# Kernel tuning notes

Measured on AMD Instinct MI355X. Metric: run time of the kernel, lower is better.

Reference implementation:

```python
import jax, jax.numpy as jnp
import numpy as np

B, S, D, H, DFF, NB = 32, 512, 256, 8, 1024, 2
L = NB + 2 * NB  # 2 blocks_1 + 4 blocks_2 = 6 layers, params stacked on axis 0
DK = D // H
NEG = jnp.float32(-1e32)


def _ln(x, s, b):
    mu = jnp.mean(x, -1, keepdims=True)
    var = jnp.mean((x - mu) ** 2, -1, keepdims=True)
    return (x - mu) * jax.lax.rsqrt(var + 1e-5) * s + b


def _attn(q, k, v, gamma, mask, zero_pad):
    # q,k,v: [B,H,S,DK]; mask: [1,1,S,S] bool; gamma: [H,1,1]
    scores = jnp.einsum('bhid,bhjd->bhij', q, k) / jnp.float32(np.sqrt(DK))
    # distance-decay effect (computed with no grad in the original)
    sc = jax.nn.softmax(jnp.where(mask, scores, NEG), axis=-1) * mask
    cum = jnp.cumsum(sc, axis=-1)
    tot = jnp.sum(sc, axis=-1, keepdims=True)
    idx = jnp.arange(S, dtype=jnp.float32)
    pos = jnp.abs(idx[None, :] - idx[:, None])[None, None]  # |i-j|
    dist = jax.lax.stop_gradient(jnp.sqrt(jnp.maximum((tot - cum) * pos, 0.0)))
    g = -jax.nn.softplus(gamma)[None]  # [1,H,1,1]
    eff = jnp.clip(jnp.exp(dist * g), 1e-5, 1e5)
    scores = jnp.where(mask, scores * eff, NEG)
    a = jax.nn.softmax(scores, axis=-1)
    if zero_pad:
        a = a.at[:, :, 0, :].set(0.0)
    return jnp.einsum('bhij,bhjd->bhid', a, v)


def _layer(i, mask_flag, q, k, v, apply_pos,
           Wk, bk, Wv, bv, Wo, bo, gammas, ln1_s, ln1_b, W1, b1, W2, b2, ln2_s, ln2_b):
    diag = 0 if mask_flag == 1 else -1  # mask=1: incl. diag; mask=0: strictly past
    mask = jnp.tril(jnp.ones((S, S), bool), diag)[None, None]
    to_h = lambda x, W, bb: (x @ W + bb).reshape(B, S, H, DK).transpose(0, 2, 1, 3)
    qh = to_h(q, Wk[i], bk[i])  # kq_same=True -> q uses k_linear
    kh = to_h(k, Wk[i], bk[i])
    vh = to_h(v, Wv[i], bv[i])
    o = _attn(qh, kh, vh, gammas[i], mask, zero_pad=(mask_flag == 0))
    o = o.transpose(0, 2, 1, 3).reshape(B, S, D) @ Wo[i] + bo[i]
    q = _ln(q + o, ln1_s[i], ln1_b[i])
    if apply_pos:
        f = jax.nn.relu(q @ W1[i] + b1[i]) @ W2[i] + b2[i]
        q = _ln(q + f, ln2_s[i], ln2_b[i])
    return q


def _forward(q_embed_data, qa_embed_data, *p):
    y, x = qa_embed_data, q_embed_data
    for i in range(NB):
        y = _layer(i, 1, y, y, y, True, *p)
    flag = True
    for j in range(2 * NB):
        i = NB + j
        if flag:
            x = _layer(i, 1, x, x, x, False, *p)
        else:
            x = _layer(i, 0, x, x, y, True, *p)
        flag = not flag
    return x


def setup_inputs() -> dict:
    key = jax.random.key(0)
    ks = jax.random.split(key, 9)
    sd = jnp.float32(1.0 / np.sqrt(D))
    sdf = jnp.float32(1.0 / np.sqrt(DFF))
    xb = float(np.sqrt(3.0))  # xavier bound for gammas (fan_in=fan_out=1)
    return {
        'q_embed_data': jax.random.normal(ks[0], (B, S, D), jnp.float32),
        'qa_embed_data': jax.random.normal(ks[1], (B, S, D), jnp.float32),
        'Wk': jax.random.normal(ks[2], (L, D, D), jnp.float32) * sd,
        'bk': jnp.zeros((L, D), jnp.float32),
        'Wv': jax.random.normal(ks[3], (L, D, D), jnp.float32) * sd,
        'bv': jnp.zeros((L, D), jnp.float32),
        'Wo': jax.random.normal(ks[4], (L, D, D), jnp.float32) * sd,
        'bo': jnp.zeros((L, D), jnp.float32),
        'gammas': jax.random.uniform(ks[5], (L, H, 1, 1), jnp.float32, -xb, xb),
        'ln1_s': jnp.ones((L, D), jnp.float32),
        'ln1_b': jnp.zeros((L, D), jnp.float32),
        'W1': jax.random.normal(ks[6], (L, D, DFF), jnp.float32) * sd,
        'b1': jnp.zeros((L, DFF), jnp.float32),
        'W2': jax.random.normal(ks[7], (L, DFF, D), jnp.float32) * sdf,
        'b2': jnp.zeros((L, D), jnp.float32),
        'ln2_s': jnp.ones((L, D), jnp.float32),
        'ln2_b': jnp.zeros((L, D), jnp.float32),
    }


def reference(q_embed_data, qa_embed_data, Wk, bk, Wv, bv, Wo, bo, gammas,
              ln1_s, ln1_b, W1, b1, W2, b2, ln2_s, ln2_b):
    return _forward(q_embed_data, qa_embed_data, Wk, bk, Wv, bv, Wo, bo, gammas,
                    ln1_s, ln1_b, W1, b1, W2, b2, ln2_s, ln2_b)
```

## Files before the change

### kernel.cpp

```cpp
#include <hip/hip_runtime.h>
#include <cstdint>
#include <cstddef>


#define AS1 __attribute__((address_space(1)))
#define AS3 __attribute__((address_space(3)))

typedef __bf16 bf16;
typedef __bf16 bf16x8 __attribute__((ext_vector_type(8)));
typedef __bf16 bf16x4 __attribute__((ext_vector_type(4)));
typedef __bf16 bf16x2 __attribute__((ext_vector_type(2)));
typedef float  f32x4  __attribute__((ext_vector_type(4)));
typedef float  f32x16 __attribute__((ext_vector_type(16)));
typedef unsigned int u32;

static constexpr int Mc = 32 * 512;

__global__ void cvt_copy2_kernel(const float* __restrict__ s0, float* __restrict__ da32,
                                 bf16* __restrict__ da16, const float* __restrict__ s1,
                                 float* __restrict__ db32, bf16* __restrict__ db16, int n4) {
  const float* s = blockIdx.y ? s1 : s0;
  float* d32 = blockIdx.y ? db32 : da32;
  bf16* d16 = blockIdx.y ? db16 : da16;
  int i = blockIdx.x * blockDim.x + threadIdx.x;
  if (i < n4) {
    float4 v = ((const float4*)s)[i];
    ((float4*)d32)[i] = v;
    bf16x4 hx = {(bf16)v.x, (bf16)v.y, (bf16)v.z, (bf16)v.w};
    ((bf16x4*)d16)[i] = hx;
  }
}

__global__ __launch_bounds__(256) void transpose_cvt_all(
    const float* __restrict__ Wk, const float* __restrict__ Wv, const float* __restrict__ Wo,
    const float* __restrict__ W1, const float* __restrict__ W2,
    bf16* __restrict__ Wkt, bf16* __restrict__ Wvt, bf16* __restrict__ Wot,
    bf16* __restrict__ W1t, bf16* __restrict__ W2t) {
  int z = blockIdx.z;
  int layer = z % 6, w = z / 6;
  const float* src; bf16* dst; int K, N;
  switch (w) {
    case 0: src = Wk; dst = Wkt; K = 256; N = 256; break;
    case 1: src = Wv; dst = Wvt; K = 256; N = 256; break;
    case 2: src = Wo; dst = Wot; K = 256; N = 256; break;
    case 3: src = W1; dst = W1t; K = 256; N = 1024; break;
    default: src = W2; dst = W2t; K = 1024; N = 256; break;
  }
  int k0 = blockIdx.x * 64, n0 = blockIdx.y * 64;
  if (k0 >= K || n0 >= N) return;
  src += (size_t)layer * K * N;
  dst += (size_t)layer * K * N;
  __shared__ bf16 t[64][68];
  int tid = threadIdx.x;
  int rr = tid >> 4;
  int c4 = (tid & 15) * 4;
#pragma unroll
  for (int p = 0; p < 4; ++p) {
    int k = rr + p * 16;
    float4 v = *(const float4*)(src + (size_t)(k0 + k) * N + n0 + c4);
    t[c4 + 0][k] = (bf16)v.x;
    t[c4 + 1][k] = (bf16)v.y;
    t[c4 + 2][k] = (bf16)v.z;
    t[c4 + 3][k] = (bf16)v.w;
  }
  __syncthreads();
#pragma unroll
  for (int p = 0; p < 4; ++p) {
    int nl = rr + p * 16;
    bf16x4 o4 = *(const bf16x4*)&t[nl][c4];
    *(bf16x4*)(dst + (size_t)(n0 + nl) * K + k0 + c4) = o4;
  }
}

template <int RELU, typename OUT_T>
__device__ __forceinline__ void gemm_body(
    const bf16* __restrict__ A, const bf16* __restrict__ Bt,
    const float* __restrict__ bias, OUT_T* __restrict__ C,
    int K, int N, int m0, int n0, bf16* As, bf16* Bs) {
  const int tid = threadIdx.x;
  const int lane = tid & 63;
  const int wid = tid >> 6;
  const int wm = (wid >> 1) * 64;
  const int wn = (wid & 1) * 64;
  f32x4 acc[4][4] = {};

  const int o1 = wid * 1024 + lane * 16;
  const int o2 = o1 + 4096;
  const int r1 = o1 >> 6, c1 = o1 & 63;
  const int r2 = o2 >> 6, c2 = o2 & 63;
  const char* Ab = (const char*)A;
  const char* Bb = (const char*)Bt;
  const size_t stride = (size_t)K * 2;

  auto stage_panel = [&](int panel, int kk) {
    const char* a1 = Ab + (size_t)(m0 + r1) * stride + (size_t)kk * 2 + c1;
    const char* a2 = Ab + (size_t)(m0 + r2) * stride + (size_t)kk * 2 + c2;
    const char* b1 = Bb + (size_t)(n0 + r1) * stride + (size_t)kk * 2 + c1;
    const char* b2 = Bb + (size_t)(n0 + r2) * stride + (size_t)kk * 2 + c2;
    char* ad = (char*)As + panel * 8192 + wid * 1024;
    char* bd = (char*)Bs + panel * 8192 + wid * 1024;
    __builtin_amdgcn_global_load_lds((const AS1 u32*)a1, (AS3 u32*)ad, 16, 0, 0);
    __builtin_amdgcn_global_load_lds((const AS1 u32*)a2, (AS3 u32*)(ad + 4096), 16, 0, 0);
    __builtin_amdgcn_global_load_lds((const AS1 u32*)b1, (AS3 u32*)bd, 16, 0, 0);
    __builtin_amdgcn_global_load_lds((const AS1 u32*)b2, (AS3 u32*)(bd + 4096), 16, 0, 0);
  };

  stage_panel(0, 0);
  stage_panel(1, 32);
  asm volatile("s_waitcnt vmcnt(0)" ::: "memory");
  __syncthreads();

  int cur = 0;
  for (int k0 = 0; k0 < K; k0 += 64) {
    if (k0 + 64 < K) {
      stage_panel((cur ^ 1) * 2, k0 + 64);
      stage_panel((cur ^ 1) * 2 + 1, k0 + 96);
    }
    const int rr = lane & 15;
    const int g8 = (lane >> 4) * 8;
#pragma unroll
    for (int s = 0; s < 2; ++s) {
      const int base = (cur * 2 + s) * 4096;
      bf16x8 af[4], bfr[4];
#pragma unroll
      for (int i = 0; i < 4; ++i) {
        af[i]  = *(const bf16x8*)&As[base + (wm + i * 16 + rr) * 32 + g8];
        bfr[i] = *(const bf16x8*)&Bs[base + (wn + i * 16 + rr) * 32 + g8];
      }
#pragma unroll
      for (int mi = 0; mi < 4; ++mi)
#pragma unroll
        for (int ni = 0; ni < 4; ++ni)
          acc[mi][ni] = __builtin_amdgcn_mfma_f32_16x16x32_bf16(af[mi], bfr[ni], acc[mi][ni], 0, 0, 0);
    }
    asm volatile("s_waitcnt vmcnt(0)" ::: "memory");
    __syncthreads();
    cur ^= 1;
  }

  const int rr = lane & 15;
  const int g4 = (lane >> 4) * 4;
  float bv[4];
#pragma unroll
  for (int ni = 0; ni < 4; ++ni) bv[ni] = bias[n0 + wn + ni * 16 + rr];
#pragma unroll
  for (int mi = 0; mi < 4; ++mi)
#pragma unroll
    for (int ni = 0; ni < 4; ++ni)
#pragma unroll
      for (int r = 0; r < 4; ++r) {
        float v = acc[mi][ni][r] + bv[ni];
        if (RELU) v = fmaxf(v, 0.f);
        int row = m0 + wm + mi * 16 + g4 + r;
        int col = n0 + wn + ni * 16 + rr;
        C[(size_t)row * N + col] = (OUT_T)v;
      }
}

template <int RELU, typename OUT_T>
__global__ __launch_bounds__(256) void gemm_bias_kernel(
    const bf16* __restrict__ A, const bf16* __restrict__ Bt,
    const float* __restrict__ bias, OUT_T* __restrict__ C, int K, int N) {
  __shared__ bf16 As[4 * 4096];
  __shared__ bf16 Bs[4 * 4096];
  gemm_body<RELU, OUT_T>(A, Bt, bias, C, K, N, blockIdx.x * 128, blockIdx.y * 128, As, Bs);
}

__global__ __launch_bounds__(256) void gemm_kv_kernel(
    const bf16* __restrict__ A0, const bf16* __restrict__ Bt0,
    const float* __restrict__ b0, bf16* __restrict__ C0,
    const bf16* __restrict__ A1, const bf16* __restrict__ Bt1,
    const float* __restrict__ b1, bf16* __restrict__ C1, int K, int N) {
  __shared__ bf16 As[4 * 4096];
  __shared__ bf16 Bs[4 * 4096];
  int sel = blockIdx.y >> 1;
  gemm_body<0, bf16>(sel ? A1 : A0, sel ? Bt1 : Bt0, sel ? b1 : b0, sel ? C1 : C0,
                     K, N, blockIdx.x * 128, (blockIdx.y & 1) * 128, As, Bs);
}

template <int KSZ>
__global__ __launch_bounds__(512, 4) void gemm_ln_kernel(
    const bf16* __restrict__ A, const bf16* __restrict__ Bt,
    const float* __restrict__ bias, const float* __restrict__ resid,
    const float* __restrict__ lns, const float* __restrict__ lnb,
    float* __restrict__ out32, bf16* __restrict__ out16) {
  __shared__ bf16 As[2 * 32 * 32];
  __shared__ bf16 Bs[2 * 256 * 32];
  __shared__ float wsum[8][16][2];
  __shared__ float stats[32][2];
  const int tid = threadIdx.x, lane = tid & 63, wid = tid >> 6;
  const int m0 = blockIdx.x * 32;
  const int wr = wid >> 2, wc = wid & 3;
  f32x4 acc[4] = {};
  const char* Ab = (const char*)A;
  const char* Bb = (const char*)Bt;
  const size_t stride = (size_t)KSZ * 2;

  auto stage = [&](int buf, int kk) {
    if (wid < 2) {
      int off = wid * 1024 + lane * 16;
      const char* a1 = Ab + (size_t)(m0 + (off >> 6)) * stride + (size_t)kk * 2 + (off & 63);
      __builtin_amdgcn_global_load_lds((const AS1 u32*)a1,
                                       (AS3 u32*)((char*)As + buf * 2048 + wid * 1024), 16, 0, 0);
    }
    int off1 = wid * 2048 + lane * 16;
    int off2 = off1 + 1024;
    const char* b1 = Bb + (size_t)(off1 >> 6) * stride + (size_t)kk * 2 + (off1 & 63);
    const char* b2 = Bb + (size_t)(off2 >> 6) * stride + (size_t)kk * 2 + (off2 & 63);
    char* bd = (char*)Bs + buf * 16384 + wid * 2048;
    __builtin_amdgcn_global_load_lds((const AS1 u32*)b1, (AS3 u32*)bd, 16, 0, 0);
    __builtin_amdgcn_global_load_lds((const AS1 u32*)b2, (AS3 u32*)(bd + 1024), 16, 0, 0);
  };

  stage(0, 0);
  asm volatile("s_waitcnt vmcnt(0)" ::: "memory");
  __syncthreads();

  int cur = 0;
  for (int k0 = 0; k0 < KSZ; k0 += 32) {
    if (k0 + 32 < KSZ) stage(cur ^ 1, k0 + 32);
    const int rr = lane & 15, g8 = (lane >> 4) * 8;
    bf16x8 af = *(const bf16x8*)&As[cur * 1024 + (wr * 16 + rr) * 32 + g8];
    bf16x8 bfr[4];
#pragma unroll
    for (int ni = 0; ni < 4; ++ni)
      bfr[ni] = *(const bf16x8*)&Bs[cur * 8192 + (wc * 64 + ni * 16 + rr) * 32 + g8];
#pragma unroll
    for (int ni = 0; ni < 4; ++ni)
      acc[ni] = __builtin_amdgcn_mfma_f32_16x16x32_bf16(af, bfr[ni], acc[ni], 0, 0, 0);
    asm volatile("s_waitcnt vmcnt(0)" ::: "memory");
    __syncthreads();
    cur ^= 1;
  }

  const int rr = lane & 15, g4 = (lane >> 4) * 4;
  float bv[4], scv[4], biv[4];
  int col[4];
#pragma unroll
  for (int ni = 0; ni < 4; ++ni) {
    col[ni] = wc * 64 + ni * 16 + rr;
    bv[ni] = bias[col[ni]];
    scv[ni] = lns[col[ni]];
    biv[ni] = lnb[col[ni]];
  }
  float v[4][4];
#pragma unroll
  for (int r = 0; r < 4; ++r) {
    int grow = m0 + wr * 16 + g4 + r;
#pragma unroll
    for (int ni = 0; ni < 4; ++ni)
      v[ni][r] = acc[ni][r] + bv[ni] + resid[(size_t)grow * 256 + col[ni]];
  }
#pragma unroll
  for (int r = 0; r < 4; ++r) {
    float s1 = (v[0][r] + v[1][r]) + (v[2][r] + v[3][r]);
    float s2 = (v[0][r] * v[0][r] + v[1][r] * v[1][r]) + (v[2][r] * v[2][r] + v[3][r] * v[3][r]);
#pragma unroll
    for (int off = 8; off; off >>= 1) {
      s1 += __shfl_xor(s1, off);
      s2 += __shfl_xor(s2, off);
    }
    if (rr == 0) {
      int lrow = wr * 16 + g4 + r;
      wsum[wid][lrow & 15][0] = s1;
      wsum[wid][lrow & 15][1] = s2;
    }
  }
  __syncthreads();
  if (tid < 32) {
    int row = tid;
    int band = row >> 4;
    float s1 = 0.f, s2 = 0.f;
#pragma unroll
    for (int k = 0; k < 4; ++k) {
      s1 += wsum[band * 4 + k][row & 15][0];
      s2 += wsum[band * 4 + k][row & 15][1];
    }
    float mu = s1 * (1.f / 256.f);
    float var = s2 * (1.f / 256.f) - mu * mu;
    stats[row][0] = mu;
    stats[row][1] = rsqrtf(var + 1e-5f);
  }
  __syncthreads();
#pragma unroll
  for (int r = 0; r < 4; ++r) {
    int lrow = wr * 16 + g4 + r;
    int grow = m0 + lrow;
    float mu = stats[lrow][0], rs = stats[lrow][1];
#pragma unroll
    for (int ni = 0; ni < 4; ++ni) {
      float y = (v[ni][r] - mu) * rs * scv[ni] + biv[ni];
      out32[(size_t)grow * 256 + col[ni]] = y;
      out16[(size_t)grow * 256 + col[ni]] = (bf16)y;
    }
  }
}

static constexpr int LDK = 34;
static constexpr int LDV = 534;
static constexpr float LOG2E = 1.4426950408889634f;
static constexpr float KSC = 0.17677669529663687f * LOG2E;

__device__ __forceinline__ int jloc(int r, int hi) { return (r & 3) + 8 * (r >> 2) + 4 * hi; }

__device__ __forceinline__ u32 pkbf(float x, float y) {
  bf16x2 t = {(bf16)x, (bf16)y};
  return __builtin_bit_cast(u32, t);
}

__device__ __forceinline__ void plswap(u32& a, u32& b) {
  asm volatile("v_permlane32_swap_b32 %0, %1" : "+v"(a), "+v"(b));
}

__device__ __forceinline__ f32x16 qk_tile(const bf16* Klds, int jbase, int lq,
                                          const bf16x8& qf0, const bf16x8& qf1, int hi) {
  const bf16x8 ka0 = *(const bf16x8*)&Klds[(jbase + lq) * LDK + hi * 8];
  const bf16x8 ka1 = *(const bf16x8*)&Klds[(jbase + lq) * LDK + 16 + hi * 8];
  f32x16 c = {};
  c = __builtin_amdgcn_mfma_f32_32x32x16_bf16(ka0, qf0, c, 0, 0, 0);
  c = __builtin_amdgcn_mfma_f32_32x32x16_bf16(ka1, qf1, c, 0, 0, 0);
  return c;
}

template <bool MASKED>
__device__ __forceinline__ void tileA(const f32x16& c, int jbase, int hi, int qlim, float& tot) {
  float t[4] = {0.f, 0.f, 0.f, 0.f};
#pragma unroll
  for (int q2 = 0; q2 < 4; ++q2)
#pragma unroll
    for (int p = 0; p < 4; ++p) {
      const int r = q2 * 4 + p;
      float e = __builtin_amdgcn_exp2f(c[r] * KSC);
      if (MASKED) {
        int j = jbase + 8 * q2 + 4 * hi + p;
        if (j > qlim) e = 0.f;
      }
      t[q2] += e;
    }
  tot += (t[0] + t[1]) + (t[2] + t[3]);
}

template <bool MASKED>
__device__ __forceinline__ void tileB(const f32x16& c, int jbase, int lq, int hi,
                                      int qlim, float itot, float gneg2, float posf,
                                      const bf16* Vt, float& run, float& sum2, f32x16& pvacc) {
  float su2[16], lcs[16], G[4];
#pragma unroll
  for (int q2 = 0; q2 < 4; ++q2) {
    float a = 0.f;
#pragma unroll
    for (int p = 0; p < 4; ++p) {
      const int r = q2 * 4 + p;
      su2[r] = c[r] * KSC;
      float e = __builtin_amdgcn_exp2f(su2[r]);
      if (MASKED) {
        int j = jbase + 8 * q2 + 4 * hi + p;
        if (j > qlim) e = 0.f;
      }
      a += e;
      lcs[r] = a;
    }
    G[q2] = a;
  }
  float Po[4];
#pragma unroll
  for (int q2 = 0; q2 < 4; ++q2) Po[q2] = __shfl_xor(G[q2], 32);
  float base[4];
  {
    float pre = run;
#pragma unroll
    for (int q2 = 0; q2 < 4; ++q2) {
      base[q2] = pre + (hi ? Po[q2] : 0.f);
      pre += G[q2] + Po[q2];
    }
    run = pre;
  }
#pragma unroll
  for (int cc = 0; cc < 2; ++cc) {
    float pv[8];
#pragma unroll
    for (int q2s = 0; q2s < 2; ++q2s) {
      const int q2 = cc * 2 + q2s;
#pragma unroll
      for (int p = 0; p < 4; ++p) {
        const int r = q2 * 4 + p;
        float cum = base[q2] + lcs[r];
        float pos = posf - (float)(8 * q2 + p);
        float d2 = fmaxf(__builtin_fmaf(-cum, itot, 1.f) * pos, 0.f);
        float dist = __builtin_amdgcn_sqrtf(d2);
        float eff = fmaxf(__builtin_amdgcn_exp2f(dist * gneg2), 1e-5f);
        float t = __builtin_amdgcn_exp2f(su2[r] * eff);
        if (MASKED) {
          int j = jbase + 8 * q2 + 4 * hi + p;
          if (j > qlim) t = 0.f;
        }
        pv[q2s * 4 + p] = t;
      }
    }
    sum2 += ((pv[0] + pv[1]) + (pv[2] + pv[3])) + ((pv[4] + pv[5]) + (pv[6] + pv[7]));
    u32 a0 = pkbf(pv[0], pv[1]);
    u32 a1 = pkbf(pv[2], pv[3]);
    u32 b0 = pkbf(pv[4], pv[5]);
    u32 b1 = pkbf(pv[6], pv[7]);
    plswap(a0, b0);
    plswap(a1, b1);
    uint4 fq; fq.x = a0; fq.y = a1; fq.z = b0; fq.w = b1;
    bf16x8 pa = __builtin_bit_cast(bf16x8, fq);
    bf16x8 vb = *(const bf16x8*)&Vt[(size_t)lq * LDV + jbase + cc * 16 + hi * 8];
    pvacc = __builtin_amdgcn_mfma_f32_32x32x16_bf16(pa, vb, pvacc, 0, 0, 0);
  }
}

__global__ __launch_bounds__(1024, 4) void attn_kernel(
    const bf16* __restrict__ kh, const bf16* __restrict__ vh,
    const float* __restrict__ gam, bf16* __restrict__ o, int incl_diag) {
  __shared__ bf16 Klds[512 * LDK];
  __shared__ bf16 Vt[32 * LDV];
  __shared__ float exA[8][32];
  __shared__ float exB[8][32];
  __shared__ float s2A[8][32];
  __shared__ float pvp[8][32][32];

  const int tid = threadIdx.x;
  const int lane = tid & 63;
  const int wid = tid >> 6;
  const int bh = blockIdx.x;
  const int b = bh >> 3, h = bh & 7;
  const bf16* kbase = kh + ((size_t)b * 4096 + h) * 32;
  const bf16* vbase = vh + ((size_t)b * 4096 + h) * 32;
  bf16* obase = o + ((size_t)b * 4096 + h) * 32;

#pragma unroll
  for (int it = 0; it < 2; ++it) {
    int t = it * 1024 + tid;
    int j = t >> 2, cc = t & 3;
    bf16x8 kv8 = *(const bf16x8*)(kbase + (size_t)j * 256 + cc * 8);
    *(bf16x8*)&Klds[j * LDK + cc * 8] = kv8;
  }
  {
    int u = tid & 255;
    int cg = tid >> 8;
    const bf16* vb = vbase + (size_t)(2 * u) * 256 + cg * 8;
    bf16x8 r0 = *(const bf16x8*)(vb);
    bf16x8 r1 = *(const bf16x8*)(vb + 256);
#pragma unroll
    for (int e = 0; e < 8; ++e) {
      bf16x2 w2 = {r0[e], r1[e]};
      *(bf16x2*)&Vt[(size_t)(cg * 8 + e) * LDV + 2 * u] = w2;
    }
  }
  __syncthreads();

  float gm = gam[h];
  float gneg = -(fmaxf(gm, 0.f) + log1pf(__expf(-fabsf(gm))));
  const float gneg2 = gneg * LOG2E;
  const int lq = lane & 31;
  const int hi = lane >> 5;

  const int p = wid & 7;
  const bool front = wid < 8;
  const int f = 7 - p;
  const int qbHi = 15 - p;
  const int ntHi = 16 - p;
  const int q0Hi = qbHi * 32;
  const int qrHi = q0Hi + lq;
  const int qlimHi = incl_diag ? qrHi : qrHi - 1;
  const int q0Lo = p * 32;
  const int qrLo = q0Lo + lq;
  const int qlimLo = incl_diag ? qrLo : qrLo - 1;

  const bf16x8 qfH0 = *(const bf16x8*)&Klds[(q0Hi + lq) * LDK + hi * 8];
  const bf16x8 qfH1 = *(const bf16x8*)&Klds[(q0Hi + lq) * LDK + 16 + hi * 8];

  float totLo = 0.f, S = 0.f;
  if (front) {
    const bf16x8 qfL0 = *(const bf16x8*)&Klds[(q0Lo + lq) * LDK + hi * 8];
    const bf16x8 qfL1 = *(const bf16x8*)&Klds[(q0Lo + lq) * LDK + 16 + hi * 8];
    for (int jt = 0; jt < p; ++jt) {
      f32x16 c = qk_tile(Klds, jt * 32, lq, qfL0, qfL1, hi);
      tileA<false>(c, jt * 32, hi, qlimLo, totLo);
    }
    {
      f32x16 c = qk_tile(Klds, q0Lo, lq, qfL0, qfL1, hi);
      tileA<true>(c, q0Lo, hi, qlimLo, totLo);
    }
    totLo += __shfl_xor(totLo, 32);
    for (int jt = 0; jt < f; ++jt) {
      f32x16 c = qk_tile(Klds, jt * 32, lq, qfH0, qfH1, hi);
      tileA<false>(c, jt * 32, hi, qlimHi, S);
    }
    S += __shfl_xor(S, 32);
    if (lane < 32) exA[p][lq] = S;
  } else {
    for (int jt = f; jt < ntHi - 1; ++jt) {
      f32x16 c = qk_tile(Klds, jt * 32, lq, qfH0, qfH1, hi);
      tileA<false>(c, jt * 32, hi, qlimHi, S);
    }
    {
      f32x16 c = qk_tile(Klds, q0Hi, lq, qfH0, qfH1, hi);
      tileA<true>(c, q0Hi, hi, qlimHi, S);
    }
    S += __shfl_xor(S, 32);
    if (lane < 32) exB[p][lq] = S;
  }
  __syncthreads();
  const float SA = exA[p][lq];
  const float SB = exB[p][lq];
  const float totHi = SA + SB;
  const float itotHi = totHi > 0.f ? 1.f / totHi : 0.f;

  f32x16 pvHi = {};
  float sum2Hi = 0.f;
  if (front) {
    const bf16x8 qfL0 = *(const bf16x8*)&Klds[(q0Lo + lq) * LDK + hi * 8];
    const bf16x8 qfL1 = *(const bf16x8*)&Klds[(q0Lo + lq) * LDK + 16 + hi * 8];
    const float itotLo = totLo > 0.f ? 1.f / totLo : 0.f;
    f32x16 pvLo = {};
    float sum2Lo = 0.f, run = 0.f;
    float posf = (float)(qrLo - 4 * hi);
    for (int jt = 0; jt < p; ++jt) {
      f32x16 c = qk_tile(Klds, jt * 32, lq, qfL0, qfL1, hi);
      tileB<false>(c, jt * 32, lq, hi, qlimLo, itotLo, gneg2, posf, Vt, run, sum2Lo, pvLo);
      posf -= 32.f;
    }
    {
      f32x16 c = qk_tile(Klds, q0Lo, lq, qfL0, qfL1, hi);
      tileB<true>(c, q0Lo, lq, hi, qlimLo, itotLo, gneg2, posf, Vt, run, sum2Lo, pvLo);
    }
    sum2Lo += __shfl_xor(sum2Lo, 32);
    const float inv2Lo = sum2Lo > 0.f ? 1.f / sum2Lo : 0.f;
#pragma unroll
    for (int r = 0; r < 16; ++r) {
      int qv = jloc(r, hi);
      float iv = __shfl(inv2Lo, qv);
      obase[(size_t)(q0Lo + qv) * 256 + lq] = (bf16)(pvLo[r] * iv);
    }
    run = 0.f;
    posf = (float)(qrHi - 4 * hi);
    for (int jt = 0; jt < f; ++jt) {
      f32x16 c = qk_tile(Klds, jt * 32, lq, qfH0, qfH1, hi);
      tileB<false>(c, jt * 32, lq, hi, qlimHi, itotHi, gneg2, posf, Vt, run, sum2Hi, pvHi);
      posf -= 32.f;
    }
    sum2Hi += __shfl_xor(sum2Hi, 32);
    if (lane < 32) s2A[p][lq] = sum2Hi;
#pragma unroll
    for (int r = 0; r < 16; ++r) pvp[p][jloc(r, hi)][lq] = pvHi[r];
  } else {
    float run = SA;
    float posf = (float)(qrHi - 4 * hi - 32 * f);
    for (int jt = f; jt < ntHi - 1; ++jt) {
      f32x16 c = qk_tile(Klds, jt * 32, lq, qfH0, qfH1, hi);
      tileB<false>(c, jt * 32, lq, hi, qlimHi, itotHi, gneg2, posf, Vt, run, sum2Hi, pvHi);
      posf -= 32.f;
    }
    {
      f32x16 c = qk_tile(Klds, q0Hi, lq, qfH0, qfH1, hi);
      tileB<true>(c, q0Hi, lq, hi, qlimHi, itotHi, gneg2, posf, Vt, run, sum2Hi, pvHi);
    }
    sum2Hi += __shfl_xor(sum2Hi, 32);
  }
  __syncthreads();
  if (!front) {
    const float s2 = s2A[p][lq] + sum2Hi;
    const float inv2 = s2 > 0.f ? 1.f / s2 : 0.f;
#pragma unroll
    for (int r = 0; r < 16; ++r) {
      int qv = jloc(r, hi);
      float iv = __shfl(inv2, qv);
      float val = pvHi[r] + pvp[p][qv][lq];
      obase[(size_t)(q0Hi + qv) * 256 + lq] = (bf16)(val * iv);
    }
  }
}

extern "C" void kernel_launch(void* const* d_in, const int* in_sizes, int n_in,
                              void* d_out, int out_size, void* d_ws, size_t ws_size,
                              hipStream_t stream) {
  const float* q_embed  = (const float*)d_in[0];
  const float* qa_embed = (const float*)d_in[1];
  const float* Wk = (const float*)d_in[2];
  const float* bk = (const float*)d_in[3];
  const float* Wv = (const float*)d_in[4];
  const float* bv = (const float*)d_in[5];
  const float* Wo = (const float*)d_in[6];
  const float* bo = (const float*)d_in[7];
  const float* gammas = (const float*)d_in[8];
  const float* ln1_s = (const float*)d_in[9];
  const float* ln1_b = (const float*)d_in[10];
  const float* W1 = (const float*)d_in[11];
  const float* b1 = (const float*)d_in[12];
  const float* W2 = (const float*)d_in[13];
  const float* b2 = (const float*)d_in[14];
  const float* ln2_s = (const float*)d_in[15];
  const float* ln2_b = (const float*)d_in[16];
  float* out = (float*)d_out;

  char* ws = (char*)d_ws;
  float* y32 = (float*)(ws);
  float* x32 = (float*)(ws + ((size_t)16 << 20));
  bf16* y16  = (bf16*)(ws + ((size_t)32 << 20));
  bf16* x16  = (bf16*)(ws + ((size_t)40 << 20));
  bf16* khb  = (bf16*)(ws + ((size_t)48 << 20));
  bf16* vhb  = (bf16*)(ws + ((size_t)56 << 20));
  bf16* o16  = (bf16*)(ws + ((size_t)64 << 20));
  bf16* h116 = (bf16*)(ws + ((size_t)88 << 20));
  bf16* Wkt  = (bf16*)(ws + ((size_t)122 << 20));
  bf16* Wvt  = Wkt + 6 * 65536;
  bf16* Wot  = Wvt + 6 * 65536;
  bf16* W1t  = Wot + 6 * 65536;
  bf16* W2t  = W1t + 6 * 262144;

  transpose_cvt_all<<<dim3(16, 16, 30), 256, 0, stream>>>(Wk, Wv, Wo, W1, W2,
                                                          Wkt, Wvt, Wot, W1t, W2t);
  cvt_copy2_kernel<<<dim3(4096, 2), 256, 0, stream>>>(q_embed, x32, x16,
                                                      qa_embed, y32, y16, Mc * 256 / 4);

  for (int i = 0; i < 6; ++i) {
    const bool first = (i < 2);
    const bool strict = (i == 3 || i == 5);
    const bool pos = first || strict;
    bf16* in16 = first ? y16 : x16;
    bf16* v16  = (first || strict) ? y16 : x16;
    float* res32 = first ? y32 : x32;

    gemm_kv_kernel<<<dim3(128, 4), 256, 0, stream>>>(
        in16, Wkt + (size_t)i * 65536, bk + i * 256, khb,
        v16, Wvt + (size_t)i * 65536, bv + i * 256, vhb, 256, 256);
    attn_kernel<<<256, 1024, 0, stream>>>(khb, vhb, gammas + i * 8, o16, strict ? 0 : 1);
    gemm_ln_kernel<256><<<512, 512, 0, stream>>>(
        o16, Wot + (size_t)i * 65536, bo + i * 256, res32,
        ln1_s + i * 256, ln1_b + i * 256, res32, in16);
    if (pos) {
      gemm_bias_kernel<1, bf16><<<dim3(128, 8), 256, 0, stream>>>(
          in16, W1t + (size_t)i * 262144, b1 + i * 1024, h116, 256, 1024);
      float* fin = (i == 5) ? out : res32;
      gemm_ln_kernel<1024><<<512, 512, 0, stream>>>(
          h116, W2t + (size_t)i * 262144, b2 + i * 256, res32,
          ln2_s + i * 256, ln2_b + i * 256, fin, in16);
    }
  }
}
```

Measured before the change: 599.1 us.

## Fuse output projection, LayerNorm and FFN1 GEMM into one kernel

Adds a kernel that computes the output projection with residual and LayerNorm for a 32-row tile. It keeps the normalized rows in LDS as bf16 and then runs the FFN first GEMM with ReLU over all 1024 columns from that LDS copy. This removes one launch per FFN layer and the re-read of the normalized activations from global memory. The trade-off is that each block now streams the whole W1 (256x1024) itself, with only 512 blocks reusing weights from cache, and the larger LDS footprint may lower occupancy.

Result: no change. 605.6 us (+1.1%).

```diff
diff --git a/kernel.cpp b/kernel.cpp
--- a/kernel.cpp
+++ b/kernel.cpp
@@ -292,6 +292,175 @@
       float y = (v[ni][r] - mu) * rs * scv[ni] + biv[ni];
       out32[(size_t)grow * 256 + col[ni]] = y;
       out16[(size_t)grow * 256 + col[ni]] = (bf16)y;
+    }
+  }
+}
+
+__global__ __launch_bounds__(512, 4) void gemm_ln_ffn1_kernel(
+    const bf16* __restrict__ A, const bf16* __restrict__ Bt,
+    const float* __restrict__ bias, const float* __restrict__ resid,
+    const float* __restrict__ lns, const float* __restrict__ lnb,
+    float* __restrict__ out32, bf16* __restrict__ out16,
+    const bf16* __restrict__ W1t, const float* __restrict__ b1,
+    bf16* __restrict__ h116) {
+  __shared__ bf16 As[2 * 32 * 32];
+  __shared__ bf16 Bs[2 * 256 * 32];
+  __shared__ bf16 vL[32 * 264];
+  __shared__ float wsum[8][16][2];
+  __shared__ float stats[32][2];
+  const int tid = threadIdx.x, lane = tid & 63, wid = tid >> 6;
+  const int m0 = blockIdx.x * 32;
+  const int wr = wid >> 2, wc = wid & 3;
+  f32x4 acc[4] = {};
+  const char* Ab = (const char*)A;
+  const char* Bb = (const char*)Bt;
+  const size_t stride = (size_t)256 * 2;
+
+  auto stage = [&](int buf, int kk) {
+    if (wid < 2) {
+      int off = wid * 1024 + lane * 16;
+      const char* a1 = Ab + (size_t)(m0 + (off >> 6)) * stride + (size_t)kk * 2 + (off & 63);
+      __builtin_amdgcn_global_load_lds((const AS1 u32*)a1,
+                                       (AS3 u32*)((char*)As + buf * 2048 + wid * 1024), 16, 0, 0);
+    }
+    int off1 = wid * 2048 + lane * 16;
+    int off2 = off1 + 1024;
+    const char* b1p = Bb + (size_t)(off1 >> 6) * stride + (size_t)kk * 2 + (off1 & 63);
+    const char* b2p = Bb + (size_t)(off2 >> 6) * stride + (size_t)kk * 2 + (off2 & 63);
+    char* bd = (char*)Bs + buf * 16384 + wid * 2048;
+    __builtin_amdgcn_global_load_lds((const AS1 u32*)b1p, (AS3 u32*)bd, 16, 0, 0);
+    __builtin_amdgcn_global_load_lds((const AS1 u32*)b2p, (AS3 u32*)(bd + 1024), 16, 0, 0);
+  };
+
+  stage(0, 0);
+  asm volatile("s_waitcnt vmcnt(0)" ::: "memory");
+  __syncthreads();
+
+  int cur = 0;
+  for (int k0 = 0; k0 < 256; k0 += 32) {
+    if (k0 + 32 < 256) stage(cur ^ 1, k0 + 32);
+    const int rr = lane & 15, g8 = (lane >> 4) * 8;
+    bf16x8 af = *(const bf16x8*)&As[cur * 1024 + (wr * 16 + rr) * 32 + g8];
+    bf16x8 bfr[4];
+#pragma unroll
+    for (int ni = 0; ni < 4; ++ni)
+      bfr[ni] = *(const bf16x8*)&Bs[cur * 8192 + (wc * 64 + ni * 16 + rr) * 32 + g8];
+#pragma unroll
+    for (int ni = 0; ni < 4; ++ni)
+      acc[ni] = __builtin_amdgcn_mfma_f32_16x16x32_bf16(af, bfr[ni], acc[ni], 0, 0, 0);
+    asm volatile("s_waitcnt vmcnt(0)" ::: "memory");
+    __syncthreads();
+    cur ^= 1;
+  }
+
+  {
+    const int rr = lane & 15, g4 = (lane >> 4) * 4;
+    float bv[4], scv[4], biv[4];
+    int col[4];
+#pragma unroll
+    for (int ni = 0; ni < 4; ++ni) {
+      col[ni] = wc * 64 + ni * 16 + rr;
+      bv[ni] = bias[col[ni]];
+      scv[ni] = lns[col[ni]];
+      biv[ni] = lnb[col[ni]];
+    }
+    float v[4][4];
+#pragma unroll
+    for (int r = 0; r < 4; ++r) {
+      int grow = m0 + wr * 16 + g4 + r;
+#pragma unroll
+      for (int ni = 0; ni < 4; ++ni)
+        v[ni][r] = acc[ni][r] + bv[ni] + resid[(size_t)grow * 256 + col[ni]];
+    }
+#pragma unroll
+    for (int r = 0; r < 4; ++r) {
+      float s1 = (v[0][r] + v[1][r]) + (v[2][r] + v[3][r]);
+      float s2 = (v[0][r] * v[0][r] + v[1][r] * v[1][r]) + (v[2][r] * v[2][r] + v[3][r] * v[3][r]);
+#pragma unroll
+      for (int off = 8; off; off >>= 1) {
+        s1 += __shfl_xor(s1, off);
+        s2 += __shfl_xor(s2, off);
+      }
+      if (rr == 0) {
+        int lrow = wr * 16 + g4 + r;
+        wsum[wid][lrow & 15][0] = s1;
+        wsum[wid][lrow & 15][1] = s2;
+      }
+    }
+    __syncthreads();
+    if (tid < 32) {
+      int row = tid;
+      int band = row >> 4;
+      float s1 = 0.f, s2 = 0.f;
+#pragma unroll
+      for (int k = 0; k < 4; ++k) {
+        s1 += wsum[band * 4 + k][row & 15][0];
+        s2 += wsum[band * 4 + k][row & 15][1];
+      }
+      float mu = s1 * (1.f / 256.f);
+      float var = s2 * (1.f / 256.f) - mu * mu;
+      stats[row][0] = mu;
+      stats[row][1] = rsqrtf(var + 1e-5f);
+    }
+    __syncthreads();
+#pragma unroll
+    for (int r = 0; r < 4; ++r) {
+      int lrow = wr * 16 + g4 + r;
+      int grow = m0 + lrow;
+      float mu = stats[lrow][0], rs = stats[lrow][1];
+#pragma unroll
+      for (int ni = 0; ni < 4; ++ni) {
+        float y = (v[ni][r] - mu) * rs * scv[ni] + biv[ni];
+        out32[(size_t)grow * 256 + col[ni]] = y;
+        out16[(size_t)grow * 256 + col[ni]] = (bf16)y;
+        vL[lrow * 264 + col[ni]] = (bf16)y;
+      }
+    }
+  }
+
+  const char* W1b = (const char*)W1t;
+  auto stage2 = [&](int buf, int nb, int kk) {
+    int off1 = wid * 2048 + lane * 16;
+    int off2 = off1 + 1024;
+    const char* b1p = W1b + (size_t)(nb * 256 + (off1 >> 6)) * stride + (size_t)kk * 2 + (off1 & 63);
+    const char* b2p = W1b + (size_t)(nb * 256 + (off2 >> 6)) * stride + (size_t)kk * 2 + (off2 & 63);
+    char* bd = (char*)Bs + buf * 16384 + wid * 2048;
+    __builtin_amdgcn_global_load_lds((const AS1 u32*)b1p, (AS3 u32*)bd, 16, 0, 0);
+    __builtin_amdgcn_global_load_lds((const AS1 u32*)b2p, (AS3 u32*)(bd + 1024), 16, 0, 0);
+  };
+
+  for (int nb = 0; nb < 4; ++nb) {
+    stage2(0, nb, 0);
+    asm volatile("s_waitcnt vmcnt(0)" ::: "memory");
+    __syncthreads();
+    f32x4 acc2[4] = {};
+    int c2 = 0;
+    for (int k0 = 0; k0 < 256; k0 += 32) {
+      if (k0 + 32 < 256) stage2(c2 ^ 1, nb, k0 + 32);
+      const int rr = lane & 15, g8 = (lane >> 4) * 8;
+      bf16x8 af = *(const bf16x8*)&vL[(wr * 16 + rr) * 264 + k0 + g8];
+      bf16x8 bfr[4];
+#pragma unroll
+      for (int ni = 0; ni < 4; ++ni)
+        bfr[ni] = *(const bf16x8*)&Bs[c2 * 8192 + (wc * 64 + ni * 16 + rr) * 32 + g8];
+#pragma unroll
+      for (int ni = 0; ni < 4; ++ni)
+        acc2[ni] = __builtin_amdgcn_mfma_f32_16x16x32_bf16(af, bfr[ni], acc2[ni], 0, 0, 0);
+      asm volatile("s_waitcnt vmcnt(0)" ::: "memory");
+      __syncthreads();
+      c2 ^= 1;
+    }
+    const int rr = lane & 15, g4 = (lane >> 4) * 4;
+#pragma unroll
+    for (int ni = 0; ni < 4; ++ni) {
+      int colh = nb * 256 + wc * 64 + ni * 16 + rr;
+      float bb = b1[colh];
+#pragma unroll
+      for (int r = 0; r < 4; ++r) {
+        int grow = m0 + wr * 16 + g4 + r;
+        float hv = fmaxf(acc2[ni][r] + bb, 0.f);
+        h116[(size_t)grow * 1024 + colh] = (bf16)hv;
+      }
     }
   }
 }
@@ -628,16 +797,19 @@
         in16, Wkt + (size_t)i * 65536, bk + i * 256, khb,
         v16, Wvt + (size_t)i * 65536, bv + i * 256, vhb, 256, 256);
     attn_kernel<<<256, 1024, 0, stream>>>(khb, vhb, gammas + i * 8, o16, strict ? 0 : 1);
-    gemm_ln_kernel<256><<<512, 512, 0, stream>>>(
-        o16, Wot + (size_t)i * 65536, bo + i * 256, res32,
-        ln1_s + i * 256, ln1_b + i * 256, res32, in16);
     if (pos) {
-      gemm_bias_kernel<1, bf16><<<dim3(128, 8), 256, 0, stream>>>(
-          in16, W1t + (size_t)i * 262144, b1 + i * 1024, h116, 256, 1024);
+      gemm_ln_ffn1_kernel<<<512, 512, 0, stream>>>(
+          o16, Wot + (size_t)i * 65536, bo + i * 256, res32,
+          ln1_s + i * 256, ln1_b + i * 256, res32, in16,
+          W1t + (size_t)i * 262144, b1 + i * 1024, h116);
       float* fin = (i == 5) ? out : res32;
       gemm_ln_kernel<1024><<<512, 512, 0, stream>>>(
           h116, W2t + (size_t)i * 262144, b2 + i * 256, res32,
           ln2_s + i * 256, ln2_b + i * 256, fin, in16);
-    }
-  }
-}
+    } else {
+      gemm_ln_kernel<256><<<512, 512, 0, stream>>>(
+          o16, Wot + (size_t)i * 65536, bo + i * 256, res32,
+          ln1_s + i * 256, ln1_b + i * 256, res32, in16);
+    }
+  }
+}
```
